# Kernel tuning notes

Hardware: AMD Instinct MI355X
Metric: run time of the kernel (lower is better)

The kernel has to match this reference:

```python
import jax, jax.numpy as jnp
from jax import lax
import numpy as np

D_MODEL = 1024
D_STATE = 16
D_CONV = 4
EXPAND = 2
D_INNER = EXPAND * D_MODEL  # 2048
BATCH = 4
SEQLEN = 2048


def setup_inputs() -> dict:
    key = jax.random.key(0)
    ks = jax.random.split(key, 8)
    s = 0.02  # small init scale for stability
    f32 = jnp.float32
    return {
        "x": jax.random.normal(ks[0], (BATCH, SEQLEN, D_MODEL), f32),
        # Linear weights stored as (in, out); torch applies x @ W.T with W (out, in) -- same math.
        "W_in": (jax.random.normal(ks[1], (D_MODEL, 2 * D_INNER), f32) * s),
        "conv_w": (jax.random.normal(ks[2], (D_INNER, 1, D_CONV), f32) * s),  # depthwise (O, I/groups=1, K)
        "conv_b": jnp.zeros((D_INNER,), f32),
        "W_xproj": (jax.random.normal(ks[3], (D_INNER, 2 * D_STATE), f32) * s),
        "W_dt": (jax.random.normal(ks[4], (D_INNER, D_INNER), f32) * s),
        "b_dt": jnp.zeros((D_INNER,), f32),
        "A_log": jnp.log(jax.random.uniform(ks[5], (D_INNER, D_STATE), f32, 1e-4, 1.0)),
        "D_param": jnp.ones((D_INNER,), f32),
        "W_out": (jax.random.normal(ks[6], (D_INNER, D_MODEL), f32) * s),
    }


def _mamba_forward(x, W_in, conv_w, conv_b, W_xproj, W_dt, b_dt, A_log, D_param, W_out):
    Bb, L, _ = x.shape
    # in_proj and split into x-branch and gate z
    xz = x @ W_in                      # (B, L, 2*d_inner)
    xc, z = jnp.split(xz, 2, axis=-1)
    # causal depthwise conv1d: torch pads both sides by d_conv-1 then slices [:L] == left-pad only
    xt = xc.transpose(0, 2, 1)         # (B, d_inner, L)
    xconv = lax.conv_general_dilated(
        xt, conv_w, window_strides=(1,), padding=[(D_CONV - 1, 0)],
        feature_group_count=D_INNER, dimension_numbers=("NCH", "OIH", "NCH"))
    xs = jax.nn.silu(xconv.transpose(0, 2, 1) + conv_b[None, None, :])  # (B, L, d_inner)
    # SSM inputs
    delta = jax.nn.softplus(xs @ W_dt + b_dt)          # (B, L, d_inner)
    Bs, Cs = jnp.split(xs @ W_xproj, 2, axis=-1)       # each (B, L, d_state)
    A = -jnp.exp(A_log)                                 # (d_inner, d_state)

    def step(h, inp):
        dt, bv, cv, xv = inp                            # (B,d_inner),(B,d_state),(B,d_state),(B,d_inner)
        dA = 1.0 + A[None] * dt[..., None]              # Euler discretization (B, d_inner, d_state)
        dB = bv[:, None, :] * (xv * dt)[..., None]
        h = h * dA + dB
        y = jnp.einsum("bds,bs->bd", h, cv) + D_param * xv
        return h, y

    inputs = (delta.transpose(1, 0, 2), Bs.transpose(1, 0, 2),
              Cs.transpose(1, 0, 2), xs.transpose(1, 0, 2))
    h0 = jnp.zeros((Bb, D_INNER, D_STATE), x.dtype)
    _, ys = lax.scan(step, h0, inputs)                  # ys: (L, B, d_inner)
    y = ys.transpose(1, 0, 2) * jax.nn.silu(z)          # gated output
    return y @ W_out                                    # (B, L, d_model)


def reference(x, W_in, conv_w, conv_b, W_xproj, W_dt, b_dt, A_log, D_param, W_out):
    return _mamba_forward(x, W_in, conv_w, conv_b, W_xproj, W_dt, b_dt, A_log, D_param, W_out)
```

## Files before the change

### kernel.cpp

```cpp
#include <hip/hip_runtime.h>

#define AS1 __attribute__((address_space(1)))
#define AS3 __attribute__((address_space(3)))

typedef unsigned short u16;
typedef __attribute__((ext_vector_type(8))) __bf16 bf16x8;
typedef __attribute__((ext_vector_type(8))) unsigned short u16x8;
typedef __attribute__((ext_vector_type(4))) float f32x4;

#define BATCH   4
#define SEQLEN  2048
#define DMODEL  1024
#define DINNER  2048
#define DSTATE  16
#define ROWS    (BATCH * SEQLEN)

__device__ __forceinline__ u16 f2bf(float f) {
  union { float f; unsigned u; } v; v.f = f;
  unsigned u = v.u;
  return (u16)((u + 0x7fffu + ((u >> 16) & 1u)) >> 16);
}
__device__ __forceinline__ float bf2f(u16 s) {
  union { unsigned u; float f; } v; v.u = ((unsigned)s) << 16;
  return v.f;
}

__global__ void cast_f32_bf16(const float* __restrict__ in, u16* __restrict__ out, int n4) {
  int i = blockIdx.x * blockDim.x + threadIdx.x;
  if (i >= n4) return;
  float4 v = ((const float4*)in)[i];
  ushort4 o;
  o.x = f2bf(v.x); o.y = f2bf(v.y); o.z = f2bf(v.z); o.w = f2bf(v.w);
  ((ushort4*)out)[i] = o;
}

__global__ void transpose_cast(const float* __restrict__ in, u16* __restrict__ out, int R, int C) {
  __shared__ float tile[32][33];
  int x  = blockIdx.x * 32 + threadIdx.x;
  int y0 = blockIdx.y * 32;
#pragma unroll
  for (int j = 0; j < 32; j += 8)
    tile[threadIdx.y + j][threadIdx.x] = in[(size_t)(y0 + threadIdx.y + j) * C + x];
  __syncthreads();
  int xo  = blockIdx.y * 32 + threadIdx.x;
  int yo0 = blockIdx.x * 32;
#pragma unroll
  for (int j = 0; j < 32; j += 8)
    out[(size_t)(yo0 + threadIdx.y + j) * R + xo] = f2bf(tile[threadIdx.x][threadIdx.y + j]);
}

template<int EPI, int BN_>
__launch_bounds__(512, 1)
__global__ void gemm8p(const u16* __restrict__ A, const u16* __restrict__ Bt,
                       void* __restrict__ outp, const float* __restrict__ bias,
                       int M, int N, int K, int gn, int rr, int cc) {
  constexpr int NF   = BN_ / 64;
  constexpr int BCH  = BN_ / 64;
  constexpr int ASZ  = 256 * 64;
  constexpr int BSZ  = BN_ * 64;
  constexpr int BUFS = ASZ + BSZ;
  extern __shared__ u16 lds[];

  const int xcd = blockIdx.x & 7, kb = blockIdx.x >> 3;
  const int tpr = gn / cc;
  const int bm  = (xcd / tpr) * rr + kb / cc;
  const int bn  = (xcd % tpr) * cc + kb % cc;

  const int tid  = threadIdx.x;
  const int wave = tid >> 6, lane = tid & 63;
  const int wm = wave >> 2, wn = wave & 3;
  const int llo = lane & 15, lhi = lane >> 4;
  const size_t bm0 = (size_t)bm * 256, bn0 = (size_t)bn * BN_;
  const int NT = K >> 6;

  const u16* gA[4];
#pragma unroll
  for (int ch = 0; ch < 4; ++ch) {
    int row  = ch * 64 + (tid >> 3);
    int scol = ((tid & 7) ^ (row & 7)) << 3;
    gA[ch] = A + (bm0 + row) * (size_t)K + scol;
  }
  const u16* gB[BCH];
#pragma unroll
  for (int ch = 0; ch < BCH; ++ch) {
    int row  = ch * 64 + (tid >> 3);
    int scol = ((tid & 7) ^ (row & 7)) << 3;
    gB[ch] = Bt + (bn0 + row) * (size_t)K + scol;
  }

  const int mask = (llo & 7) << 4;
  const int ko[2] = { ((0 + lhi * 16) ^ mask) >> 1, ((64 + lhi * 16) ^ mask) >> 1 };

#define SGA(t, bsel, ch) __builtin_amdgcn_global_load_lds(                       \
    (const AS1 void*)(gA[ch] + ((size_t)(t) << 6)),                              \
    (AS3 void*)(lds + (bsel) * BUFS + (ch) * 4096 + wave * 512), 16, 0, 0)
#define SGB(t, bsel, ch) __builtin_amdgcn_global_load_lds(                       \
    (const AS1 void*)(gB[ch] + ((size_t)(t) << 6)),                              \
    (AS3 void*)(lds + (bsel) * BUFS + ASZ + (ch) * 4096 + wave * 512), 16, 0, 0)

  f32x4 acc[8][NF] = {};
  bf16x8 bfr[2][NF];

#define PHASE(la_, lb_, MH, KK, RDB, STG, WC)                                    \
  {                                                                              \
    bf16x8 af[4];                                                                \
    _Pragma("unroll") for (int m = 0; m < 4; ++m)                                \
      af[m] = *(const bf16x8*)(const void*)((la_) + (wm*128 + MH*64 + m*16 + llo)*64 + ko[KK]); \
    if (RDB) {                                                                   \
      _Pragma("unroll") for (int n = 0; n < NF; ++n)                             \
        bfr[KK][n] = *(const bf16x8*)(const void*)((lb_) + (wn*(16*NF) + n*16 + llo)*64 + ko[KK]); \
    }                                                                            \
    STG;                                                                         \
    __builtin_amdgcn_s_barrier();                                                \
    __builtin_amdgcn_s_setprio(1);                                               \
    _Pragma("unroll") for (int m = 0; m < 4; ++m)                                \
      _Pragma("unroll") for (int n = 0; n < NF; ++n)                             \
        acc[MH*4+m][n] = __builtin_amdgcn_mfma_f32_16x16x32_bf16(af[m], bfr[KK][n], acc[MH*4+m][n], 0, 0, 0); \
    __builtin_amdgcn_s_setprio(0);                                               \
    WC;                                                                          \
    __builtin_amdgcn_s_barrier();                                                \
  }

  SGA(0, 0, 0); SGA(0, 0, 2); SGB(0, 0, 0); SGB(0, 0, 1);
  if (BCH == 4) { SGB(0, 0, 2); SGB(0, 0, 3); }
  SGA(0, 0, 1); SGA(0, 0, 3);
  SGA(1, 1, 0); SGA(1, 1, 2); SGB(1, 1, 0); SGB(1, 1, 1);
  asm volatile("s_waitcnt vmcnt(4)" ::: "memory");
  __builtin_amdgcn_s_barrier();

  const u16* la0 = lds;            const u16* lb0 = lds + ASZ;
  const u16* la1 = lds + BUFS;     const u16* lb1 = la1 + ASZ;

  for (int u = 0; u < NT; u += 2) {
    const int v = u + 1;
    PHASE(la0, lb0, 0, 0, true,
          ({ if (BCH == 4) { SGB(v, 1, 2); SGB(v, 1, 3); } else { SGA(v, 1, 1); SGA(v, 1, 3); } }),
          ((void)0));
    PHASE(la0, lb0, 0, 1, true,
          ({ if (BCH == 4) { SGA(v, 1, 1); SGA(v, 1, 3); } }),
          ((void)0));
    PHASE(la0, lb0, 1, 0, false,
          ({ if (u + 2 < NT) { SGA(u + 2, 0, 0); SGA(u + 2, 0, 2); } }),
          ((void)0));
    PHASE(la0, lb0, 1, 1, false,
          ({ if (u + 2 < NT) { SGB(u + 2, 0, 0); SGB(u + 2, 0, 1); } }),
          ({ if (u + 2 < NT) asm volatile("s_waitcnt vmcnt(4)" ::: "memory");
             else            asm volatile("s_waitcnt vmcnt(0)" ::: "memory"); }));
    PHASE(la1, lb1, 0, 0, true,
          ({ if (u + 2 < NT) { if (BCH == 4) { SGB(u + 2, 0, 2); SGB(u + 2, 0, 3); }
                               else          { SGA(u + 2, 0, 1); SGA(u + 2, 0, 3); } } }),
          ((void)0));
    PHASE(la1, lb1, 0, 1, true,
          ({ if (u + 2 < NT && BCH == 4) { SGA(u + 2, 0, 1); SGA(u + 2, 0, 3); } }),
          ((void)0));
    PHASE(la1, lb1, 1, 0, false,
          ({ if (v + 2 < NT) { SGA(v + 2, 1, 0); SGA(v + 2, 1, 2); } }),
          ((void)0));
    PHASE(la1, lb1, 1, 1, false,
          ({ if (v + 2 < NT) { SGB(v + 2, 1, 0); SGB(v + 2, 1, 1); } }),
          ({ if (v + 2 < NT) asm volatile("s_waitcnt vmcnt(4)" ::: "memory");
             else            asm volatile("s_waitcnt vmcnt(0)" ::: "memory"); }));
  }
#undef PHASE
#undef SGA
#undef SGB

#pragma unroll
  for (int am = 0; am < 8; ++am) {
    const int mh = am >> 2, m = am & 3;
    const int rowb = (int)bm0 + wm * 128 + mh * 64 + m * 16 + lhi * 4;
#pragma unroll
    for (int n = 0; n < NF; ++n) {
      const int col = (int)bn0 + wn * (16 * NF) + n * 16 + llo;
#pragma unroll
      for (int r = 0; r < 4; ++r) {
        float v = acc[am][n][r];
        size_t idx = (size_t)(rowb + r) * N + col;
        if (EPI == 0) {
          ((u16*)outp)[idx] = f2bf(v);
        } else if (EPI == 1) {
          float xb = v + bias[col];
          float sp = (xb > 20.f) ? xb : log1pf(__expf(xb));
          ((u16*)outp)[idx] = f2bf(sp);
        } else {
          ((float*)outp)[idx] = v;
        }
      }
    }
  }
}

__global__ void conv_silu(const u16* __restrict__ xz, const float* __restrict__ w,
                          const float* __restrict__ cb, u16* __restrict__ xs, int total) {
  int idx = blockIdx.x * 256 + threadIdx.x;
  if (idx >= total) return;
  int d = idx & (DINNER - 1);
  int l = (idx >> 11) & (SEQLEN - 1);
  int b = idx >> 22;
  float4 wv = ((const float4*)w)[d];
  float acc = cb[d];
#pragma unroll
  for (int k = 0; k < 4; ++k) {
    int li = l - 3 + k;
    if (li >= 0) {
      float xv = bf2f(xz[(size_t)(b * SEQLEN + li) * (2 * DINNER) + d]);
      acc = fmaf((&wv.x)[k], xv, acc);
    }
  }
  float s = acc / (1.f + __expf(-acc));
  xs[(size_t)idx] = f2bf(s);
}

__global__ void xproj_kernel(const u16* __restrict__ xs, const float* __restrict__ Wx,
                             float* __restrict__ outp) {
  __shared__ float part[256];
  int row = blockIdx.x;
  int tid = threadIdx.x;
  int c = tid & 31, kp = tid >> 5;
  const u16* xr = xs + (size_t)row * DINNER + kp * 256;
  const float* wp = Wx + (size_t)(kp * 256) * 32 + c;
  float acc = 0.f;
#pragma unroll 4
  for (int kk = 0; kk < 32; ++kk) {
    u16x8 xv = *(const u16x8*)(const void*)(xr + kk * 8);
#pragma unroll
    for (int j = 0; j < 8; ++j)
      acc = fmaf(bf2f(xv[j]), wp[(kk * 8 + j) * 32], acc);
  }
  part[tid] = acc;
  __syncthreads();
  if (tid < 32) {
    float s = 0.f;
#pragma unroll
    for (int p = 0; p < 8; ++p) s += part[p * 32 + tid];
    outp[(size_t)row * 32 + tid] = s;
  }
}

#define SC_NC 32
#define SC_CL (SEQLEN / SC_NC)
#define SC_DG 16

__launch_bounds__(512, 2)
__global__ void scan_chunked(const u16* __restrict__ delta, const u16* __restrict__ xs,
                             const float* __restrict__ xproj, const u16* __restrict__ xz,
                             const float* __restrict__ A_log, const float* __restrict__ Dp,
                             u16* __restrict__ yg) {
  __shared__ float cP[SC_NC][SC_DG][DSTATE];
  __shared__ float cH[SC_NC][SC_DG][DSTATE];
  const int tid = threadIdx.x;
  const int dl = tid & 15, ck = tid >> 4;
  const int b = blockIdx.x >> 7, dblk = blockIdx.x & 127;
  const int d = dblk * SC_DG + dl;
  const int r0 = b * SEQLEN + ck * SC_CL;

  float A[DSTATE];
  {
    const f32x4* ap = (const f32x4*)(A_log + (size_t)d * DSTATE);
#pragma unroll
    for (int q = 0; q < 4; ++q) {
      f32x4 a = ap[q];
#pragma unroll
      for (int j = 0; j < 4; ++j) A[q * 4 + j] = -__expf(a[j]);
    }
  }

  float P[DSTATE], Hh[DSTATE];
#pragma unroll
  for (int s = 0; s < DSTATE; ++s) { P[s] = 1.f; Hh[s] = 0.f; }
#pragma unroll 2
  for (int l = 0; l < SC_CL; ++l) {
    size_t row = (size_t)(r0 + l);
    float dt = bf2f(delta[row * DINNER + d]);
    float xv = bf2f(xs[row * DINNER + d]);
    float dtx = dt * xv;
    const f32x4* bp = (const f32x4*)(xproj + row * 32);
    f32x4 Bq[4];
#pragma unroll
    for (int q = 0; q < 4; ++q) Bq[q] = bp[q];
#pragma unroll
    for (int s = 0; s < DSTATE; ++s) {
      float dA = fmaf(A[s], dt, 1.f);
      P[s] *= dA;
      Hh[s] = fmaf(Hh[s], dA, Bq[s >> 2][s & 3] * dtx);
    }
  }
#pragma unroll
  for (int s = 0; s < DSTATE; ++s) { cP[ck][dl][s] = P[s]; cH[ck][dl][s] = Hh[s]; }
  __syncthreads();

  if (tid < SC_DG * DSTATE) {
    int s2 = tid & 15, dd = tid >> 4;
    float h = 0.f;
    for (int c = 0; c < SC_NC; ++c) {
      float p = cP[c][dd][s2], hh = cH[c][dd][s2];
      cP[c][dd][s2] = h;
      h = fmaf(p, h, hh);
    }
  }
  __syncthreads();

  float h[DSTATE];
#pragma unroll
  for (int s = 0; s < DSTATE; ++s) h[s] = cP[ck][dl][s];
  const float Dv = Dp[d];
#pragma unroll 2
  for (int l = 0; l < SC_CL; ++l) {
    size_t row = (size_t)(r0 + l);
    float dt = bf2f(delta[row * DINNER + d]);
    float xv = bf2f(xs[row * DINNER + d]);
    float dtx = dt * xv;
    const f32x4* bp = (const f32x4*)(xproj + row * 32);
    f32x4 Bq[4], Cq[4];
#pragma unroll
    for (int q = 0; q < 4; ++q) { Bq[q] = bp[q]; Cq[q] = bp[q + 4]; }
    float yp = 0.f;
#pragma unroll
    for (int s = 0; s < DSTATE; ++s) {
      float dA = fmaf(A[s], dt, 1.f);
      h[s] = fmaf(h[s], dA, Bq[s >> 2][s & 3] * dtx);
      yp = fmaf(h[s], Cq[s >> 2][s & 3], yp);
    }
    float z = bf2f(xz[row * (2 * DINNER) + DINNER + d]);
    float y = yp + Dv * xv;
    float g = z / (1.f + __expf(-z));
    yg[row * DINNER + d] = f2bf(y * g);
  }
}

extern "C" void kernel_launch(void* const* d_in, const int* in_sizes, int n_in,
                              void* d_out, int out_size, void* d_ws, size_t ws_size,
                              hipStream_t stream) {
  const float* x       = (const float*)d_in[0];
  const float* W_in    = (const float*)d_in[1];
  const float* conv_w  = (const float*)d_in[2];
  const float* conv_b  = (const float*)d_in[3];
  const float* W_xproj = (const float*)d_in[4];
  const float* W_dt    = (const float*)d_in[5];
  const float* b_dt    = (const float*)d_in[6];
  const float* A_log   = (const float*)d_in[7];
  const float* D_param = (const float*)d_in[8];
  const float* W_out   = (const float*)d_in[9];
  float* out = (float*)d_out;

  char* ws = (char*)d_ws;
  const size_t MB = 1ull << 20;
  u16*   x_bf  = (u16*)(ws);
  u16*   WinT  = (u16*)(ws + 16 * MB);
  u16*   WdtT  = (u16*)(ws + 24 * MB);
  u16*   xz_bf = (u16*)(ws + 32 * MB);
  u16*   xs_bf = (u16*)(ws + 96 * MB);
  u16*   delta = (u16*)(ws + 128 * MB);
  float* xpj   = (float*)(ws + 192 * MB);
  u16*   WoutT = (u16*)(ws + 193 * MB);
  u16*   yg    = (u16*)(ws);

  hipFuncSetAttribute((const void*)gemm8p<0, 256>, hipFuncAttributeMaxDynamicSharedMemorySize, 131072);
  hipFuncSetAttribute((const void*)gemm8p<1, 256>, hipFuncAttributeMaxDynamicSharedMemorySize, 131072);
  hipFuncSetAttribute((const void*)gemm8p<2, 128>, hipFuncAttributeMaxDynamicSharedMemorySize, 98304);

  dim3 tb(32, 8);

  cast_f32_bf16<<<(ROWS * DMODEL / 4 + 255) / 256, 256, 0, stream>>>(x, x_bf, ROWS * DMODEL / 4);
  transpose_cast<<<dim3((2 * DINNER) / 32, DMODEL / 32), tb, 0, stream>>>(W_in, WinT, DMODEL, 2 * DINNER);
  transpose_cast<<<dim3(DINNER / 32, DINNER / 32), tb, 0, stream>>>(W_dt, WdtT, DINNER, DINNER);
  transpose_cast<<<dim3(DMODEL / 32, DINNER / 32), tb, 0, stream>>>(W_out, WoutT, DINNER, DMODEL);

  gemm8p<0, 256><<<512, 512, 131072, stream>>>(x_bf, WinT, xz_bf, nullptr,
                                               ROWS, 2 * DINNER, DMODEL, 16, 8, 8);

  conv_silu<<<(ROWS * DINNER) / 256, 256, 0, stream>>>(xz_bf, conv_w, conv_b, xs_bf, ROWS * DINNER);

  gemm8p<1, 256><<<256, 512, 131072, stream>>>(xs_bf, WdtT, delta, b_dt,
                                               ROWS, DINNER, DINNER, 8, 4, 8);

  xproj_kernel<<<ROWS, 256, 0, stream>>>(xs_bf, W_xproj, xpj);

  scan_chunked<<<BATCH * (DINNER / SC_DG), 512, 0, stream>>>(
      delta, xs_bf, xpj, xz_bf, A_log, D_param, yg);

  gemm8p<2, 128><<<256, 512, 98304, stream>>>(yg, WoutT, out, nullptr,
                                              ROWS, DMODEL, DINNER, 8, 4, 8);
}
```

Measured before the change: 513.0 us.

## Vectorize conv-silu and process two channels per thread in chunked scan

The conv+SiLU kernel now handles four channels per thread with vector loads and stores. The chunked scan is restructured so each thread owns two adjacent channels, reading packed bf16 pairs and sharing the B/C loads. It also software-prefetches the next rows' delta, x, z and B/C values and pads the LDS carry arrays to avoid bank conflicts. This cuts global load instructions and redundant xproj reads but doubles per-thread register state, lowering occupancy (launch bounds 512,1) and halving the number of blocks.

```diff
diff --git a/kernel.cpp b/kernel.cpp
--- a/kernel.cpp
+++ b/kernel.cpp
@@ -4,6 +4,7 @@
 #define AS3 __attribute__((address_space(3)))
 
 typedef unsigned short u16;
+typedef unsigned int u32;
 typedef __attribute__((ext_vector_type(8))) __bf16 bf16x8;
 typedef __attribute__((ext_vector_type(8))) unsigned short u16x8;
 typedef __attribute__((ext_vector_type(4))) float f32x4;
@@ -24,6 +25,8 @@
   union { unsigned u; float f; } v; v.u = ((unsigned)s) << 16;
   return v.f;
 }
+__device__ __forceinline__ float bflo(u32 p) { union { unsigned u; float f; } v; v.u = p << 16; return v.f; }
+__device__ __forceinline__ float bfhi(u32 p) { union { unsigned u; float f; } v; v.u = p & 0xffff0000u; return v.f; }
 
 __global__ void cast_f32_bf16(const float* __restrict__ in, u16* __restrict__ out, int n4) {
   int i = blockIdx.x * blockDim.x + threadIdx.x;
@@ -190,25 +193,36 @@
   }
 }
 
-__global__ void conv_silu(const u16* __restrict__ xz, const float* __restrict__ w,
-                          const float* __restrict__ cb, u16* __restrict__ xs, int total) {
+__global__ void conv_silu4(const u16* __restrict__ xz, const float* __restrict__ w,
+                           const float* __restrict__ cb, u16* __restrict__ xs, int total4) {
   int idx = blockIdx.x * 256 + threadIdx.x;
-  if (idx >= total) return;
-  int d = idx & (DINNER - 1);
-  int l = (idx >> 11) & (SEQLEN - 1);
-  int b = idx >> 22;
-  float4 wv = ((const float4*)w)[d];
-  float acc = cb[d];
+  if (idx >= total4) return;
+  int d4 = idx & (DINNER / 4 - 1);
+  int l  = (idx >> 9) & (SEQLEN - 1);
+  int b  = idx >> 20;
+  int d  = d4 * 4;
+  float4 wv[4];
+#pragma unroll
+  for (int j = 0; j < 4; ++j) wv[j] = ((const float4*)w)[d + j];
+  float4 bias = *(const float4*)(cb + d);
+  float acc[4] = { bias.x, bias.y, bias.z, bias.w };
 #pragma unroll
   for (int k = 0; k < 4; ++k) {
     int li = l - 3 + k;
     if (li >= 0) {
-      float xv = bf2f(xz[(size_t)(b * SEQLEN + li) * (2 * DINNER) + d]);
-      acc = fmaf((&wv.x)[k], xv, acc);
-    }
-  }
-  float s = acc / (1.f + __expf(-acc));
-  xs[(size_t)idx] = f2bf(s);
+      ushort4 xv = *(const ushort4*)(xz + (size_t)(b * SEQLEN + li) * (2 * DINNER) + d);
+      acc[0] = fmaf((&wv[0].x)[k], bf2f(xv.x), acc[0]);
+      acc[1] = fmaf((&wv[1].x)[k], bf2f(xv.y), acc[1]);
+      acc[2] = fmaf((&wv[2].x)[k], bf2f(xv.z), acc[2]);
+      acc[3] = fmaf((&wv[3].x)[k], bf2f(xv.w), acc[3]);
+    }
+  }
+  ushort4 o;
+  o.x = f2bf(acc[0] / (1.f + __expf(-acc[0])));
+  o.y = f2bf(acc[1] / (1.f + __expf(-acc[1])));
+  o.z = f2bf(acc[2] / (1.f + __expf(-acc[2])));
+  o.w = f2bf(acc[3] / (1.f + __expf(-acc[3])));
+  *(ushort4*)(xs + (size_t)idx * 4) = o;
 }
 
 __global__ void xproj_kernel(const u16* __restrict__ xs, const float* __restrict__ Wx,
@@ -238,93 +252,145 @@
 }
 
 #define SC_NC 32
-#define SC_CL (SEQLEN / SC_NC)
-#define SC_DG 16
-
-__launch_bounds__(512, 2)
-__global__ void scan_chunked(const u16* __restrict__ delta, const u16* __restrict__ xs,
-                             const float* __restrict__ xproj, const u16* __restrict__ xz,
-                             const float* __restrict__ A_log, const float* __restrict__ Dp,
-                             u16* __restrict__ yg) {
-  __shared__ float cP[SC_NC][SC_DG][DSTATE];
-  __shared__ float cH[SC_NC][SC_DG][DSTATE];
+#define SC_CL 64
+#define SC_LDS (2 * SC_NC * 16 * 33 * 4)
+
+__launch_bounds__(512, 1)
+__global__ void scan_v3(const u16* __restrict__ delta, const u16* __restrict__ xs,
+                        const float* __restrict__ xproj, const u16* __restrict__ xz,
+                        const float* __restrict__ A_log, const float* __restrict__ Dp,
+                        u16* __restrict__ yg) {
+  extern __shared__ float smem[];
+  float* cP = smem;
+  float* cH = smem + SC_NC * 16 * 33;
   const int tid = threadIdx.x;
   const int dl = tid & 15, ck = tid >> 4;
-  const int b = blockIdx.x >> 7, dblk = blockIdx.x & 127;
-  const int d = dblk * SC_DG + dl;
+  const int b = blockIdx.x >> 6, dblk = blockIdx.x & 63;
+  const int d0 = dblk * 32 + dl * 2;
   const int r0 = b * SEQLEN + ck * SC_CL;
 
-  float A[DSTATE];
-  {
-    const f32x4* ap = (const f32x4*)(A_log + (size_t)d * DSTATE);
+  float A0[DSTATE], A1[DSTATE];
+  {
+    const f32x4* ap0 = (const f32x4*)(A_log + (size_t)d0 * DSTATE);
+    const f32x4* ap1 = (const f32x4*)(A_log + (size_t)(d0 + 1) * DSTATE);
 #pragma unroll
     for (int q = 0; q < 4; ++q) {
-      f32x4 a = ap[q];
-#pragma unroll
-      for (int j = 0; j < 4; ++j) A[q * 4 + j] = -__expf(a[j]);
-    }
-  }
-
-  float P[DSTATE], Hh[DSTATE];
-#pragma unroll
-  for (int s = 0; s < DSTATE; ++s) { P[s] = 1.f; Hh[s] = 0.f; }
-#pragma unroll 2
-  for (int l = 0; l < SC_CL; ++l) {
-    size_t row = (size_t)(r0 + l);
-    float dt = bf2f(delta[row * DINNER + d]);
-    float xv = bf2f(xs[row * DINNER + d]);
-    float dtx = dt * xv;
-    const f32x4* bp = (const f32x4*)(xproj + row * 32);
-    f32x4 Bq[4];
-#pragma unroll
-    for (int q = 0; q < 4; ++q) Bq[q] = bp[q];
+      f32x4 a0 = ap0[q], a1 = ap1[q];
+#pragma unroll
+      for (int j = 0; j < 4; ++j) { A0[q * 4 + j] = -__expf(a0[j]); A1[q * 4 + j] = -__expf(a1[j]); }
+    }
+  }
+
+  const u32* dP = (const u32*)(delta + (size_t)r0 * DINNER + d0);
+  const u32* xP = (const u32*)(xs    + (size_t)r0 * DINNER + d0);
+  const u32* zP = (const u32*)(xz + (size_t)r0 * (2 * DINNER) + DINNER + d0);
+  const float* bP = xproj + (size_t)r0 * 32;
+  const int DW = DINNER / 2;
+  const int ZW = DINNER;
+
+  float P0[DSTATE], P1[DSTATE], H0[DSTATE], H1[DSTATE];
+#pragma unroll
+  for (int s = 0; s < DSTATE; ++s) { P0[s] = P1[s] = 1.f; H0[s] = H1[s] = 0.f; }
+  {
+    u32 dq0 = dP[0], xq0 = xP[0];
+    u32 dq1 = dP[DW], xq1 = xP[DW];
+    f32x4 Bn[4];
+#pragma unroll
+    for (int q = 0; q < 4; ++q) Bn[q] = ((const f32x4*)bP)[q];
+    for (int l = 0; l < SC_CL; ++l) {
+      const u32 dc = dq0, xc = xq0;
+      dq0 = dq1; xq0 = xq1;
+      if (l + 2 < SC_CL) { dq1 = dP[(l + 2) * DW]; xq1 = xP[(l + 2) * DW]; }
+      f32x4 Bc[4] = { Bn[0], Bn[1], Bn[2], Bn[3] };
+      if (l + 1 < SC_CL) {
+        const f32x4* bn = (const f32x4*)(bP + (l + 1) * 32);
+#pragma unroll
+        for (int q = 0; q < 4; ++q) Bn[q] = bn[q];
+      }
+      float dt0 = bflo(dc), dt1 = bfhi(dc);
+      float x0 = bflo(xc),  x1 = bfhi(xc);
+      float dtx0 = dt0 * x0, dtx1 = dt1 * x1;
+#pragma unroll
+      for (int s = 0; s < DSTATE; ++s) {
+        float bs = Bc[s >> 2][s & 3];
+        float dA0 = fmaf(A0[s], dt0, 1.f);
+        float dA1 = fmaf(A1[s], dt1, 1.f);
+        P0[s] *= dA0; P1[s] *= dA1;
+        H0[s] = fmaf(H0[s], dA0, bs * dtx0);
+        H1[s] = fmaf(H1[s], dA1, bs * dtx1);
+      }
+    }
+  }
+  {
+    float* p = cP + (ck * 16 + dl) * 33;
+    float* h = cH + (ck * 16 + dl) * 33;
 #pragma unroll
     for (int s = 0; s < DSTATE; ++s) {
-      float dA = fmaf(A[s], dt, 1.f);
-      P[s] *= dA;
-      Hh[s] = fmaf(Hh[s], dA, Bq[s >> 2][s & 3] * dtx);
-    }
-  }
-#pragma unroll
-  for (int s = 0; s < DSTATE; ++s) { cP[ck][dl][s] = P[s]; cH[ck][dl][s] = Hh[s]; }
+      p[s] = P0[s]; p[16 + s] = P1[s];
+      h[s] = H0[s]; h[16 + s] = H1[s];
+    }
+  }
   __syncthreads();
 
-  if (tid < SC_DG * DSTATE) {
-    int s2 = tid & 15, dd = tid >> 4;
+  {
+    const int s2 = tid & 15, dd = tid >> 4;
+    const int idx = (dd & 1) * 16 + s2;
+    float* pbase = cP + (dd >> 1) * 33 + idx;
+    float* hbase = cH + (dd >> 1) * 33 + idx;
     float h = 0.f;
     for (int c = 0; c < SC_NC; ++c) {
-      float p = cP[c][dd][s2], hh = cH[c][dd][s2];
-      cP[c][dd][s2] = h;
+      float p = pbase[c * 16 * 33], hh = hbase[c * 16 * 33];
+      pbase[c * 16 * 33] = h;
       h = fmaf(p, h, hh);
     }
   }
   __syncthreads();
 
-  float h[DSTATE];
-#pragma unroll
-  for (int s = 0; s < DSTATE; ++s) h[s] = cP[ck][dl][s];
-  const float Dv = Dp[d];
-#pragma unroll 2
-  for (int l = 0; l < SC_CL; ++l) {
-    size_t row = (size_t)(r0 + l);
-    float dt = bf2f(delta[row * DINNER + d]);
-    float xv = bf2f(xs[row * DINNER + d]);
-    float dtx = dt * xv;
-    const f32x4* bp = (const f32x4*)(xproj + row * 32);
-    f32x4 Bq[4], Cq[4];
-#pragma unroll
-    for (int q = 0; q < 4; ++q) { Bq[q] = bp[q]; Cq[q] = bp[q + 4]; }
-    float yp = 0.f;
-#pragma unroll
-    for (int s = 0; s < DSTATE; ++s) {
-      float dA = fmaf(A[s], dt, 1.f);
-      h[s] = fmaf(h[s], dA, Bq[s >> 2][s & 3] * dtx);
-      yp = fmaf(h[s], Cq[s >> 2][s & 3], yp);
-    }
-    float z = bf2f(xz[row * (2 * DINNER) + DINNER + d]);
-    float y = yp + Dv * xv;
-    float g = z / (1.f + __expf(-z));
-    yg[row * DINNER + d] = f2bf(y * g);
+  float h0[DSTATE], h1[DSTATE];
+  {
+    const float* p = cP + (ck * 16 + dl) * 33;
+#pragma unroll
+    for (int s = 0; s < DSTATE; ++s) { h0[s] = p[s]; h1[s] = p[16 + s]; }
+  }
+  const float Dv0 = Dp[d0], Dv1 = Dp[d0 + 1];
+  u32* yP = (u32*)(yg + (size_t)r0 * DINNER + d0);
+  {
+    u32 dq0 = dP[0], xq0 = xP[0], zq0 = zP[0];
+    u32 dq1 = dP[DW], xq1 = xP[DW], zq1 = zP[ZW];
+    f32x4 Bn[4], Cn[4];
+#pragma unroll
+    for (int q = 0; q < 4; ++q) { Bn[q] = ((const f32x4*)bP)[q]; Cn[q] = ((const f32x4*)bP)[q + 4]; }
+    for (int l = 0; l < SC_CL; ++l) {
+      const u32 dc = dq0, xc = xq0, zc = zq0;
+      dq0 = dq1; xq0 = xq1; zq0 = zq1;
+      if (l + 2 < SC_CL) { dq1 = dP[(l + 2) * DW]; xq1 = xP[(l + 2) * DW]; zq1 = zP[(l + 2) * ZW]; }
+      f32x4 Bc[4] = { Bn[0], Bn[1], Bn[2], Bn[3] };
+      f32x4 Cc[4] = { Cn[0], Cn[1], Cn[2], Cn[3] };
+      if (l + 1 < SC_CL) {
+        const f32x4* bn = (const f32x4*)(bP + (l + 1) * 32);
+#pragma unroll
+        for (int q = 0; q < 4; ++q) { Bn[q] = bn[q]; Cn[q] = bn[q + 4]; }
+      }
+      float dt0 = bflo(dc), dt1 = bfhi(dc);
+      float x0 = bflo(xc),  x1 = bfhi(xc);
+      float dtx0 = dt0 * x0, dtx1 = dt1 * x1;
+      float yp0 = 0.f, yp1 = 0.f;
+#pragma unroll
+      for (int s = 0; s < DSTATE; ++s) {
+        float bs = Bc[s >> 2][s & 3];
+        float cs = Cc[s >> 2][s & 3];
+        float dA0 = fmaf(A0[s], dt0, 1.f);
+        float dA1 = fmaf(A1[s], dt1, 1.f);
+        h0[s] = fmaf(h0[s], dA0, bs * dtx0);
+        h1[s] = fmaf(h1[s], dA1, bs * dtx1);
+        yp0 = fmaf(h0[s], cs, yp0);
+        yp1 = fmaf(h1[s], cs, yp1);
+      }
+      float z0 = bflo(zc), z1 = bfhi(zc);
+      float y0 = (yp0 + Dv0 * x0) * (z0 / (1.f + __expf(-z0)));
+      float y1 = (yp1 + Dv1 * x1) * (z1 / (1.f + __expf(-z1)));
+      yP[l * DW] = (u32)f2bf(y0) | ((u32)f2bf(y1) << 16);
+    }
   }
 }
 
@@ -358,6 +424,7 @@
   hipFuncSetAttribute((const void*)gemm8p<0, 256>, hipFuncAttributeMaxDynamicSharedMemorySize, 131072);
   hipFuncSetAttribute((const void*)gemm8p<1, 256>, hipFuncAttributeMaxDynamicSharedMemorySize, 131072);
   hipFuncSetAttribute((const void*)gemm8p<2, 128>, hipFuncAttributeMaxDynamicSharedMemorySize, 98304);
+  hipFuncSetAttribute((const void*)scan_v3, hipFuncAttributeMaxDynamicSharedMemorySize, SC_LDS);
 
   dim3 tb(32, 8);
 
@@ -369,14 +436,15 @@
   gemm8p<0, 256><<<512, 512, 131072, stream>>>(x_bf, WinT, xz_bf, nullptr,
                                                ROWS, 2 * DINNER, DMODEL, 16, 8, 8);
 
-  conv_silu<<<(ROWS * DINNER) / 256, 256, 0, stream>>>(xz_bf, conv_w, conv_b, xs_bf, ROWS * DINNER);
+  conv_silu4<<<(ROWS * DINNER / 4) / 256, 256, 0, stream>>>(
+      xz_bf, conv_w, conv_b, xs_bf, ROWS * DINNER / 4);
 
   gemm8p<1, 256><<<256, 512, 131072, stream>>>(xs_bf, WdtT, delta, b_dt,
                                                ROWS, DINNER, DINNER, 8, 4, 8);
 
   xproj_kernel<<<ROWS, 256, 0, stream>>>(xs_bf, W_xproj, xpj);
 
-  scan_chunked<<<BATCH * (DINNER / SC_DG), 512, 0, stream>>>(
+  scan_v3<<<BATCH * (DINNER / 32), 512, SC_LDS, stream>>>(
       delta, xs_bf, xpj, xz_bf, A_log, D_param, yg);
 
   gemm8p<2, 128><<<256, 512, 98304, stream>>>(yg, WoutT, out, nullptr,
```

Measured after the change: 476.5 us. 1.08x faster.
